# Kernel optimization log

Hardware: AMD Instinct MI355X
Metric: run time of the kernel (lower is better)

The kernel has to match this reference:

```python
import jax, jax.numpy as jnp
import numpy as np


def setup_inputs() -> dict:
    key = jax.random.key(0)
    k1, k2, k3, k4 = jax.random.split(key, 4)
    B, T, H = 4, 512, 256
    scale = 1.0 / np.sqrt(H)
    return {
        "rnn_outputs": jax.random.normal(k1, (B, T, H), dtype=jnp.float32),
        "W1": jax.random.normal(k2, (H, H), dtype=jnp.float32) * scale,
        "W2": jax.random.normal(k3, (H, H), dtype=jnp.float32) * scale,
        "v": jax.random.normal(k4, (H,), dtype=jnp.float32) * scale,
    }


def reference(rnn_outputs, W1, W2, v):
    """Bahdanau additive self-attention with causal mask.

    rnn_outputs: (B, T, H). Returns (context (B,T,H), weights (B,T,T)).
    """
    B, T, H = rnn_outputs.shape
    # nn.Linear applies x @ W.T
    query = rnn_outputs @ W1.T            # (B, T, H)
    keys = rnn_outputs @ W2.T             # (B, T, H)
    # scores[b,t,s] = v . tanh(q[b,t] + k[b,s]); materializes (B,T,T,H) like the original
    scores = jnp.einsum(
        "btsh,h->bts", jnp.tanh(query[:, :, None, :] + keys[:, None, :, :]), v
    )
    causal = jnp.triu(jnp.ones((T, T), dtype=bool), k=1)  # mask future positions
    scores = jnp.where(causal[None], -jnp.inf, scores)
    weights = jax.nn.softmax(scores, axis=-1)
    weights = jnp.nan_to_num(weights)
    context = jnp.einsum("bts,bsh->bth", weights, rnn_outputs)
    return context, weights
```

## Files before the change

kernel.cpp:

```cpp
#include <hip/hip_runtime.h>

namespace {

constexpr int kB = 4;
constexpr int kT = 512;
constexpr int kH = 256;

__device__ __forceinline__ float rcpf(float x) {
  return __builtin_amdgcn_rcpf(x);
}

__global__ __launch_bounds__(256) void transpose_w_kernel(
    const float* __restrict__ W1, const float* __restrict__ W2,
    float* __restrict__ Wt1, float* __restrict__ Wt2) {
  __shared__ float tile[32][33];
  const float* Win = (blockIdx.z == 0) ? W1 : W2;
  float* Wout = (blockIdx.z == 0) ? Wt1 : Wt2;
  const int jo = blockIdx.x * 32, ho = blockIdx.y * 32;
  const int c = threadIdx.x & 31, r0 = threadIdx.x >> 5;
#pragma unroll
  for (int p = 0; p < 4; ++p)
    tile[r0 + 8 * p][c] = Win[(size_t)(ho + r0 + 8 * p) * kH + jo + c];
  __syncthreads();
#pragma unroll
  for (int p = 0; p < 4; ++p)
    Wout[(size_t)(jo + r0 + 8 * p) * kH + ho + c] = tile[c][r0 + 8 * p];
}

__global__ __launch_bounds__(256) void proj_kernel(
    const float* __restrict__ X, const float* __restrict__ Wt1,
    const float* __restrict__ Wt2, float* __restrict__ EQt,
    float* __restrict__ EKt) {
  __shared__ __align__(16) float xs[8 * kH];
  __shared__ __align__(16) float ws4[4][8][kH];

  const int tid = threadIdx.x;
  const int w = tid >> 6, lane = tid & 63;
  const int row0 = blockIdx.x * 8;
  const float* Wt = (blockIdx.y == 0) ? Wt1 : Wt2;
  float* dst = (blockIdx.y == 0) ? EQt : EKt;

  {
    const float* gx = X + (size_t)row0 * kH + w * 512 + lane * 4;
    __builtin_amdgcn_global_load_lds(
        (const __attribute__((address_space(1))) void*)gx,
        (__attribute__((address_space(3))) void*)(xs + w * 512), 16, 0, 0);
    __builtin_amdgcn_global_load_lds(
        (const __attribute__((address_space(1))) void*)(gx + 256),
        (__attribute__((address_space(3))) void*)(xs + w * 512 + 256), 16, 0,
        0);
  }

  const float* gwA = Wt + (size_t)(2 * w) * kH + lane * 4;
  const float* gwB = gwA + kH;

#define PSTAGE(buf, c)                                                        \
  {                                                                           \
    const size_t go = (size_t)(c) * 8 * kH;                                   \
    __builtin_amdgcn_global_load_lds(                                         \
        (const __attribute__((address_space(1))) void*)(gwA + go),            \
        (__attribute__((address_space(3))) void*)&ws4[buf][2 * w][0], 16, 0,  \
        0);                                                                   \
    __builtin_amdgcn_global_load_lds(                                         \
        (const __attribute__((address_space(1))) void*)(gwB + go),            \
        (__attribute__((address_space(3))) void*)&ws4[buf][2 * w + 1][0], 16, \
        0, 0);                                                                \
  }

  PSTAGE(0, 0)
  PSTAGE(1, 1)
  PSTAGE(2, 2)

  float acc[8];
#pragma unroll
  for (int i = 0; i < 8; ++i) acc[i] = 0.0f;

#pragma unroll 1
  for (int c = 0; c < 32; ++c) {
    if (c <= 29) {
      asm volatile("s_waitcnt vmcnt(4)" ::: "memory");
    } else if (c == 30) {
      asm volatile("s_waitcnt vmcnt(2)" ::: "memory");
    } else {
      asm volatile("s_waitcnt vmcnt(0)" ::: "memory");
    }
    __builtin_amdgcn_s_barrier();
    __builtin_amdgcn_sched_barrier(0);
    if (c <= 28) PSTAGE((c + 3) & 3, c + 3)
    const int bf = c & 3;

    float xr[8][8];
#pragma unroll
    for (int i = 0; i < 8; ++i) {
      const float4 a = *reinterpret_cast<const float4*>(&xs[i * kH + c * 8]);
      const float4 bx =
          *reinterpret_cast<const float4*>(&xs[i * kH + c * 8 + 4]);
      xr[i][0] = a.x;  xr[i][1] = a.y;  xr[i][2] = a.z;  xr[i][3] = a.w;
      xr[i][4] = bx.x; xr[i][5] = bx.y; xr[i][6] = bx.z; xr[i][7] = bx.w;
    }
#pragma unroll
    for (int u = 0; u < 8; ++u) {
      const float wv = ws4[bf][u][tid];
#pragma unroll
      for (int i = 0; i < 8; ++i)
        acc[i] = __builtin_fmaf(xr[i][u], wv, acc[i]);
    }
  }
#undef PSTAGE

  const int bb = row0 >> 9, r0 = row0 & (kT - 1);
  float* out = dst + ((size_t)(bb * kH + tid)) * kT + r0;
  float4 lo = {__expf(2.0f * acc[0]), __expf(2.0f * acc[1]),
               __expf(2.0f * acc[2]), __expf(2.0f * acc[3])};
  float4 hi = {__expf(2.0f * acc[4]), __expf(2.0f * acc[5]),
               __expf(2.0f * acc[6]), __expf(2.0f * acc[7])};
  *reinterpret_cast<float4*>(out) = lo;
  *reinterpret_cast<float4*>(out + 4) = hi;
}

__global__ __launch_bounds__(256) void score_kernel(
    const float* __restrict__ EQt, const float* __restrict__ EKt,
    const float* __restrict__ v, float* __restrict__ Sc) {
  __shared__ __align__(16) float eqs[4][32 * 32];
  __shared__ __align__(16) float eks[4][32 * 32];

  const int tid = threadIdx.x;
  const int w = tid >> 6, lane = tid & 63;
  const int blk = blockIdx.x;
  const int xcd = blk & 7;
  const int b = xcd >> 1;
  const int tIdx = (xcd & 1) * 68 + (blk >> 3);

  int ti = (int)((__builtin_sqrtf(8.0f * (float)tIdx + 1.0f) - 1.0f) * 0.5f);
  while ((ti + 1) * (ti + 2) / 2 <= tIdx) ++ti;
  while (ti * (ti + 1) / 2 > tIdx) --ti;
  const int si = tIdx - ti * (ti + 1) / 2;
  const int t0 = ti * 32, s0 = si * 32;

  const int hoff = w * 8 + (lane >> 3);
  const int coff = (lane & 7) * 4;
  const float* gq = EQt + ((size_t)(b * kH + hoff) * kT) + t0 + coff;
  const float* gk = EKt + ((size_t)(b * kH + hoff) * kT) + s0 + coff;
  float* lqw = &eqs[0][0] + w * 256;
  float* lkw = &eks[0][0] + w * 256;

#define STAGE(buf, c)                                                        \
  {                                                                          \
    const size_t go = (size_t)(c) * 32 * kT;                                 \
    __builtin_amdgcn_global_load_lds(                                        \
        (const __attribute__((address_space(1))) void*)(gq + go),            \
        (__attribute__((address_space(3))) void*)(lqw + (buf)*1024), 16, 0,  \
        0);                                                                  \
    __builtin_amdgcn_global_load_lds(                                        \
        (const __attribute__((address_space(1))) void*)(gk + go),            \
        (__attribute__((address_space(3))) void*)(lkw + (buf)*1024), 16, 0,  \
        0);                                                                  \
  }

  const int wt = w >> 1, wsx = w & 1;
  const int tq = wt * 16 + 2 * (lane >> 3);
  const int sk = wsx * 16 + 2 * (lane & 7);

  float ac0 = 0.f, ac1 = 0.f, ac2 = 0.f, ac3 = 0.f;
  float ac4 = 0.f, ac5 = 0.f, ac6 = 0.f, ac7 = 0.f;

  STAGE(0, 0)
  STAGE(1, 1)
  STAGE(2, 2)

#pragma unroll 1
  for (int c = 0; c < 8; ++c) {
    if (c <= 5) {
      asm volatile("s_waitcnt vmcnt(4)" ::: "memory");
    } else if (c == 6) {
      asm volatile("s_waitcnt vmcnt(2)" ::: "memory");
    } else {
      asm volatile("s_waitcnt vmcnt(0)" ::: "memory");
    }
    __builtin_amdgcn_s_barrier();
    __builtin_amdgcn_sched_barrier(0);
    if (c <= 4) STAGE((c + 3) & 3, c + 3)
    const int boff = (c & 3) * 1024;
    const float* vp = v + c * 32;
#pragma unroll
    for (int h = 0; h < 32; h += 2) {
      const float2 qA = *reinterpret_cast<const float2*>(&eqs[0][boff + h * 32 + tq]);
      const float2 kA = *reinterpret_cast<const float2*>(&eks[0][boff + h * 32 + sk]);
      const float2 qB = *reinterpret_cast<const float2*>(&eqs[0][boff + h * 32 + 32 + tq]);
      const float2 kB = *reinterpret_cast<const float2*>(&eks[0][boff + h * 32 + 32 + sk]);
      const float vA = vp[h], vB = vp[h + 1];
      ac0 = __builtin_fmaf(vA, rcpf(__builtin_fmaf(qA.x, kA.x, 1.0f)), ac0);
      ac1 = __builtin_fmaf(vA, rcpf(__builtin_fmaf(qA.x, kA.y, 1.0f)), ac1);
      ac2 = __builtin_fmaf(vA, rcpf(__builtin_fmaf(qA.y, kA.x, 1.0f)), ac2);
      ac3 = __builtin_fmaf(vA, rcpf(__builtin_fmaf(qA.y, kA.y, 1.0f)), ac3);
      ac4 = __builtin_fmaf(vB, rcpf(__builtin_fmaf(qB.x, kB.x, 1.0f)), ac4);
      ac5 = __builtin_fmaf(vB, rcpf(__builtin_fmaf(qB.x, kB.y, 1.0f)), ac5);
      ac6 = __builtin_fmaf(vB, rcpf(__builtin_fmaf(qB.y, kB.x, 1.0f)), ac6);
      ac7 = __builtin_fmaf(vB, rcpf(__builtin_fmaf(qB.y, kB.y, 1.0f)), ac7);
    }
  }
#undef STAGE

  float vv = v[lane] + v[lane + 64] + v[lane + 128] + v[lane + 192];
#pragma unroll
  for (int off = 32; off > 0; off >>= 1) vv += __shfl_xor(vv, off, 64);

  float2 row0v = {__builtin_fmaf(-2.0f, ac0 + ac4, vv),
                  __builtin_fmaf(-2.0f, ac1 + ac5, vv)};
  float2 row1v = {__builtin_fmaf(-2.0f, ac2 + ac6, vv),
                  __builtin_fmaf(-2.0f, ac3 + ac7, vv)};
  float* so = Sc + ((size_t)(b * kT + t0 + tq)) * kT + s0 + sk;
  *reinterpret_cast<float2*>(so) = row0v;
  *reinterpret_cast<float2*>(so + kT) = row1v;
}

__global__ __launch_bounds__(512) void attn2_kernel(
    const float* __restrict__ X, float* wsc, float* __restrict__ ctx) {
  __shared__ float wls[8][kT + 8];
  __shared__ float pc[2][8][kH];

  const int id = blockIdx.x;
  const int xcd = id & 7;
  const int b = xcd >> 1;
  const int sub = (xcd & 1) * 32 + (id >> 3);
  const int row0 = sub * 8;
  const int tid = threadIdx.x;
  const int w = tid >> 6, lane = tid & 63;

  const int t = row0 + w;
  float* srow = wsc + ((size_t)(b * kT + t)) * kT;
  const int sbase8 = lane * 8;
  float4 s4a = *reinterpret_cast<const float4*>(srow + sbase8);
  float4 s4b = *reinterpret_cast<const float4*>(srow + sbase8 + 4);
  float p[8];
  p[0] = (sbase8 + 0 <= t) ? __expf(s4a.x) : 0.f;
  p[1] = (sbase8 + 1 <= t) ? __expf(s4a.y) : 0.f;
  p[2] = (sbase8 + 2 <= t) ? __expf(s4a.z) : 0.f;
  p[3] = (sbase8 + 3 <= t) ? __expf(s4a.w) : 0.f;
  p[4] = (sbase8 + 4 <= t) ? __expf(s4b.x) : 0.f;
  p[5] = (sbase8 + 5 <= t) ? __expf(s4b.y) : 0.f;
  p[6] = (sbase8 + 6 <= t) ? __expf(s4b.z) : 0.f;
  p[7] = (sbase8 + 7 <= t) ? __expf(s4b.w) : 0.f;
  float l = ((p[0] + p[1]) + (p[2] + p[3])) + ((p[4] + p[5]) + (p[6] + p[7]));
#pragma unroll
  for (int off = 32; off > 0; off >>= 1) l += __shfl_xor(l, off, 64);
  const float rs = rcpf(l);
#pragma unroll
  for (int j = 0; j < 8; ++j) p[j] *= rs;
  float4 o4a = {p[0], p[1], p[2], p[3]};
  float4 o4b = {p[4], p[5], p[6], p[7]};
  *reinterpret_cast<float4*>(srow + sbase8) = o4a;
  *reinterpret_cast<float4*>(srow + sbase8 + 4) = o4b;
#pragma unroll
  for (int j = 0; j < 8; ++j) wls[w][sbase8 + j] = p[j];
  __syncthreads();

  const int h = tid & (kH - 1);
  const int half = tid >> 8;
  const float* Xb = X + ((size_t)b * kT) * kH + h;
  float acc[8];
#pragma unroll
  for (int r = 0; r < 8; ++r) acc[r] = 0.f;
  const int sb = half * 256;
#pragma unroll 2
  for (int so = 0; so < 256; so += 4) {
    const int s = sb + so;
    const float x0 = Xb[(size_t)(s + 0) * kH];
    const float x1 = Xb[(size_t)(s + 1) * kH];
    const float x2 = Xb[(size_t)(s + 2) * kH];
    const float x3 = Xb[(size_t)(s + 3) * kH];
#pragma unroll
    for (int r = 0; r < 8; ++r) {
      const float4 wr = *reinterpret_cast<const float4*>(&wls[r][s]);
      float a = __builtin_fmaf(wr.x, x0, acc[r]);
      a = __builtin_fmaf(wr.y, x1, a);
      a = __builtin_fmaf(wr.z, x2, a);
      acc[r] = __builtin_fmaf(wr.w, x3, a);
    }
  }
#pragma unroll
  for (int r = 0; r < 8; ++r) pc[half][r][h] = acc[r];
  __syncthreads();

#pragma unroll
  for (int q = 0; q < 4; ++q) {
    const int idx = q * 512 + tid;
    const int r = idx >> 8, hh = idx & (kH - 1);
    ctx[((size_t)(b * kT + row0 + r)) * kH + hh] = pc[0][r][hh] + pc[1][r][hh];
  }
}

}

extern "C" void kernel_launch(void* const* d_in, const int* in_sizes, int n_in,
                              void* d_out, int out_size, void* d_ws,
                              size_t ws_size, hipStream_t stream) {
  const float* X = (const float*)d_in[0];
  const float* W1 = (const float*)d_in[1];
  const float* W2 = (const float*)d_in[2];
  const float* v = (const float*)d_in[3];

  float* ctx = (float*)d_out;
  float* wout = ctx + (size_t)kB * kT * kH;
  float* Wt1 = wout;
  float* Wt2 = wout + (size_t)kH * kH;
  float* Sc = wout;
  float* EQt = (float*)d_ws;
  float* EKt = EQt + (size_t)kB * kH * kT;

  transpose_w_kernel<<<dim3(8, 8, 2), 256, 0, stream>>>(W1, W2, Wt1, Wt2);
  proj_kernel<<<dim3(kB * kT / 8, 2), 256, 0, stream>>>(X, Wt1, Wt2, EQt, EKt);
  score_kernel<<<544, 256, 0, stream>>>(EQt, EKt, v, Sc);
  attn2_kernel<<<256, 512, 0, stream>>>(X, Sc, ctx);
}
```

Before: 75.45 us.

## Split score kernel H-chunks across 8 waves and simplify context loop

The score kernel goes from 256 to 512 threads. Four waves now stage Q and four stage K, each issuing one load per stage. The two wave halves split each 32-wide H chunk into two 16-wide halves, and their partial sums are combined through LDS before the store. The aim is more parallelism per tile and shorter dependent reciprocal/FMA chains, at the cost of an extra reduction, more barriers and idle waves during the final write. Separately, the context loop in attn2 drops the 4-wide float4 unrolling and uses a scalar per-s loop with unroll 4.

```diff
diff --git a/kernel.cpp b/kernel.cpp
--- a/kernel.cpp
+++ b/kernel.cpp
@@ -118,7 +118,7 @@
   *reinterpret_cast<float4*>(out + 4) = hi;
 }
 
-__global__ __launch_bounds__(256) void score_kernel(
+__global__ __launch_bounds__(512) void score_kernel(
     const float* __restrict__ EQt, const float* __restrict__ EKt,
     const float* __restrict__ v, float* __restrict__ Sc) {
   __shared__ __align__(16) float eqs[4][32 * 32];
@@ -137,27 +137,24 @@
   const int si = tIdx - ti * (ti + 1) / 2;
   const int t0 = ti * 32, s0 = si * 32;
 
-  const int hoff = w * 8 + (lane >> 3);
+  const int sw = w & 3;
+  const int hoff = sw * 8 + (lane >> 3);
   const int coff = (lane & 7) * 4;
-  const float* gq = EQt + ((size_t)(b * kH + hoff) * kT) + t0 + coff;
-  const float* gk = EKt + ((size_t)(b * kH + hoff) * kT) + s0 + coff;
-  float* lqw = &eqs[0][0] + w * 256;
-  float* lkw = &eks[0][0] + w * 256;
-
-#define STAGE(buf, c)                                                        \
-  {                                                                          \
-    const size_t go = (size_t)(c) * 32 * kT;                                 \
-    __builtin_amdgcn_global_load_lds(                                        \
-        (const __attribute__((address_space(1))) void*)(gq + go),            \
-        (__attribute__((address_space(3))) void*)(lqw + (buf)*1024), 16, 0,  \
-        0);                                                                  \
-    __builtin_amdgcn_global_load_lds(                                        \
-        (const __attribute__((address_space(1))) void*)(gk + go),            \
-        (__attribute__((address_space(3))) void*)(lkw + (buf)*1024), 16, 0,  \
-        0);                                                                  \
-  }
-
-  const int wt = w >> 1, wsx = w & 1;
+  const bool isK = w >= 4;
+  const float* gsrc = (isK ? EKt : EQt) + ((size_t)(b * kH + hoff) * kT) +
+                      (isK ? s0 : t0) + coff;
+  float* ldst = (isK ? &eks[0][0] : &eqs[0][0]) + sw * 256;
+
+#define STAGE(buf, c)                                                      \
+  __builtin_amdgcn_global_load_lds(                                        \
+      (const __attribute__((address_space(1))) void*)(gsrc +               \
+                                                      (size_t)(c)*32 * kT),\
+      (__attribute__((address_space(3))) void*)(ldst + (buf)*1024), 16, 0, \
+      0);
+
+  const int q = w & 3;
+  const int hh = w >> 2;
+  const int wt = q >> 1, wsx = q & 1;
   const int tq = wt * 16 + 2 * (lane >> 3);
   const int sk = wsx * 16 + 2 * (lane & 7);
 
@@ -171,19 +168,19 @@
 #pragma unroll 1
   for (int c = 0; c < 8; ++c) {
     if (c <= 5) {
-      asm volatile("s_waitcnt vmcnt(4)" ::: "memory");
+      asm volatile("s_waitcnt vmcnt(2)" ::: "memory");
     } else if (c == 6) {
-      asm volatile("s_waitcnt vmcnt(2)" ::: "memory");
+      asm volatile("s_waitcnt vmcnt(1)" ::: "memory");
     } else {
       asm volatile("s_waitcnt vmcnt(0)" ::: "memory");
     }
     __builtin_amdgcn_s_barrier();
     __builtin_amdgcn_sched_barrier(0);
     if (c <= 4) STAGE((c + 3) & 3, c + 3)
-    const int boff = (c & 3) * 1024;
-    const float* vp = v + c * 32;
-#pragma unroll
-    for (int h = 0; h < 32; h += 2) {
+    const int boff = (c & 3) * 1024 + hh * 512;
+    const float* vp = v + c * 32 + hh * 16;
+#pragma unroll
+    for (int h = 0; h < 16; h += 2) {
       const float2 qA = *reinterpret_cast<const float2*>(&eqs[0][boff + h * 32 + tq]);
       const float2 kA = *reinterpret_cast<const float2*>(&eks[0][boff + h * 32 + sk]);
       const float2 qB = *reinterpret_cast<const float2*>(&eqs[0][boff + h * 32 + 32 + tq]);
@@ -201,17 +198,32 @@
   }
 #undef STAGE
 
-  float vv = v[lane] + v[lane + 64] + v[lane + 128] + v[lane + 192];
-#pragma unroll
-  for (int off = 32; off > 0; off >>= 1) vv += __shfl_xor(vv, off, 64);
-
-  float2 row0v = {__builtin_fmaf(-2.0f, ac0 + ac4, vv),
-                  __builtin_fmaf(-2.0f, ac1 + ac5, vv)};
-  float2 row1v = {__builtin_fmaf(-2.0f, ac2 + ac6, vv),
-                  __builtin_fmaf(-2.0f, ac3 + ac7, vv)};
-  float* so = Sc + ((size_t)(b * kT + t0 + tq)) * kT + s0 + sk;
-  *reinterpret_cast<float2*>(so) = row0v;
-  *reinterpret_cast<float2*>(so + kT) = row1v;
+  float r00 = ac0 + ac4, r01 = ac1 + ac5;
+  float r10 = ac2 + ac6, r11 = ac3 + ac7;
+
+  float* cmb = &eqs[0][0];
+  __syncthreads();
+  if (hh == 1) {
+    float4 pv = {r00, r01, r10, r11};
+    *reinterpret_cast<float4*>(&cmb[q * 256 + lane * 4]) = pv;
+  }
+  __syncthreads();
+  if (hh == 0) {
+    const float4 pv = *reinterpret_cast<const float4*>(&cmb[q * 256 + lane * 4]);
+    r00 += pv.x; r01 += pv.y; r10 += pv.z; r11 += pv.w;
+
+    float vv = v[lane] + v[lane + 64] + v[lane + 128] + v[lane + 192];
+#pragma unroll
+    for (int off = 32; off > 0; off >>= 1) vv += __shfl_xor(vv, off, 64);
+
+    float2 row0v = {__builtin_fmaf(-2.0f, r00, vv),
+                    __builtin_fmaf(-2.0f, r01, vv)};
+    float2 row1v = {__builtin_fmaf(-2.0f, r10, vv),
+                    __builtin_fmaf(-2.0f, r11, vv)};
+    float* so = Sc + ((size_t)(b * kT + t0 + tq)) * kT + s0 + sk;
+    *reinterpret_cast<float2*>(so) = row0v;
+    *reinterpret_cast<float2*>(so + kT) = row1v;
+  }
 }
 
 __global__ __launch_bounds__(512) void attn2_kernel(
@@ -262,21 +274,13 @@
 #pragma unroll
   for (int r = 0; r < 8; ++r) acc[r] = 0.f;
   const int sb = half * 256;
-#pragma unroll 2
-  for (int so = 0; so < 256; so += 4) {
+#pragma unroll 4
+  for (int so = 0; so < 256; ++so) {
     const int s = sb + so;
-    const float x0 = Xb[(size_t)(s + 0) * kH];
-    const float x1 = Xb[(size_t)(s + 1) * kH];
-    const float x2 = Xb[(size_t)(s + 2) * kH];
-    const float x3 = Xb[(size_t)(s + 3) * kH];
-#pragma unroll
-    for (int r = 0; r < 8; ++r) {
-      const float4 wr = *reinterpret_cast<const float4*>(&wls[r][s]);
-      float a = __builtin_fmaf(wr.x, x0, acc[r]);
-      a = __builtin_fmaf(wr.y, x1, a);
-      a = __builtin_fmaf(wr.z, x2, a);
-      acc[r] = __builtin_fmaf(wr.w, x3, a);
-    }
+    const float x = Xb[(size_t)s * kH];
+#pragma unroll
+    for (int r = 0; r < 8; ++r)
+      acc[r] = __builtin_fmaf(wls[r][s], x, acc[r]);
   }
 #pragma unroll
   for (int r = 0; r < 8; ++r) pc[half][r][h] = acc[r];
@@ -310,6 +314,6 @@
 
   transpose_w_kernel<<<dim3(8, 8, 2), 256, 0, stream>>>(W1, W2, Wt1, Wt2);
   proj_kernel<<<dim3(kB * kT / 8, 2), 256, 0, stream>>>(X, Wt1, Wt2, EQt, EKt);
-  score_kernel<<<544, 256, 0, stream>>>(EQt, EKt, v, Sc);
+  score_kernel<<<544, 512, 0, stream>>>(EQt, EKt, v, Sc);
   attn2_kernel<<<256, 512, 0, stream>>>(X, Sc, ctx);
 }
```

Result: slower. 77.65 us (+2.9%).
